# Optimization experiments

Hardware: AMD Instinct MI355X
Metric: run time of the kernel (lower is better)

The kernel has to match this reference:

```python
import jax, jax.numpy as jnp
import numpy as np

C_IN, C_OUT, H = 8, 8, 16
N1D = 20                      # 1D quadrature points -> 400 mesh nodes in 2D
B = 16
DECAY = (N1D / 4.0) ** 4      # set_quad: decay_param = (N/4)**4


def _quad_mesh():
    # Gauss-Legendre nodes/weights on [-1,1], tensor-product in 2D (get_quad_mesh)
    x, w = np.polynomial.legendre.leggauss(N1D)
    X, Y = np.meshgrid(x, x, indexing='xy')
    WX, WY = np.meshgrid(w, w, indexing='xy')
    nodes = np.dstack([X, Y]).reshape(-1, 2).astype(np.float32)
    weights = (WX * WY).reshape(-1).astype(np.float32)
    return nodes, weights


def setup_inputs() -> dict:
    key = jax.random.key(0)
    k1, k2, k3, k4 = jax.random.split(key, 4)
    nodes, w = _quad_mesh()
    K = C_IN * C_OUT
    return {
        'features': jax.random.normal(k1, (B, C_IN, N1D * N1D), jnp.float32),
        # 64 tiny MLPs (Linear no bias + Sin), spec (2,16,16,1), stacked on axis 0
        'W1': jax.random.normal(k2, (K, H, 2), jnp.float32) / np.sqrt(2.0),
        'W2': jax.random.normal(k3, (K, H, H), jnp.float32) / np.sqrt(float(H)),
        'W3': jax.random.normal(k4, (K, 1, H), jnp.float32) / np.sqrt(float(H)),
        'output_locs': jnp.asarray(nodes),   # (M,2) same tensor-product mesh
        'mesh_nodes': jnp.asarray(nodes),    # (N,2)
        'mesh_weights': jnp.asarray(w),      # (N,) product of 1D weights
    }


def _kernel(W1, W2, W3, output_locs, mesh_nodes):
    # pairwise eval points z = y_m - x_n, shape (M, N, 2)
    z = output_locs[:, None, :] - mesh_nodes[None, :, :]
    M, N, _ = z.shape
    zf = z.reshape(M * N, 2)
    # batched tiny MLPs: Linear -> Sin -> Linear -> Sin -> Linear (no bias)
    h = jnp.sin(jnp.einsum('khd,pd->kph', W1, zf))
    h = jnp.sin(jnp.einsum('koh,kph->kpo', W2, h))
    kv = jnp.einsum('koh,kph->kpo', W3, h)[..., 0]          # (K, M*N)
    # bump function enforcing compact support: exp(1 - 1/(1 - c*||z||^4))
    bump_arg = jnp.sum(zf * zf, axis=-1) ** 2               # ||z||^4
    inside = bump_arg < 1.0 / DECAY
    safe = jnp.where(inside, 1.0 - DECAY * bump_arg, 1.0)
    bump = jnp.where(inside, jnp.exp(1.0 - 1.0 / safe), 0.0)
    kv = kv * bump[None, :]
    return kv.reshape(C_OUT, C_IN, M, N)


def reference(features, W1, W2, W3, output_locs, mesh_nodes, mesh_weights):
    Kmat = _kernel(W1, W2, W3, output_locs, mesh_nodes)     # (Co,Ci,M,N)
    # quadrature-weighted conv sum: out[b,o,m] = sum_{i,n} K[o,i,m,n] w[n] f[b,i,n]
    return jnp.einsum('oimn,n,bin->bom', Kmat, mesh_weights, features)
```

## Files before the change

kernel.cpp:

```cpp
#include <hip/hip_runtime.h>
#include <math.h>

#define CIN   8
#define COUT  8
#define HH    16
#define NN    400
#define MM    400
#define BB    16

#define THREADS 512
#define GM      2
#define PMAX    32

#define WS_FT 0
#define WS_L  (NN*CIN*BB)

__global__ __launch_bounds__(THREADS) void prep_kernel(
    const float* __restrict__ f,
    const float* __restrict__ locs,
    const float* __restrict__ nodes,
    const float* __restrict__ wq,
    float* __restrict__ ws)
{
    const int blk = blockIdx.x;
    const int t   = threadIdx.x;

    if (blk < 100) {
        int idx = blk * 512 + t;
        int b = idx / 3200;
        int r = idx - b * 3200;
        int i = r / 400;
        int n = r - i * 400;
        ws[WS_FT + n*128 + i*16 + b] = f[idx];
    } else {
        const int lane = t & 63;
        const int w    = t >> 6;
        const int m    = (blk - 100) * 8 + w;
        const float2 y = ((const float2*)locs)[m];
        const float2* nd = (const float2*)nodes;
        float4* lst = (float4*)(ws + WS_L);
        int cnt = 0;
        for (int n0 = 0; n0 < NN; n0 += 64) {
            int n = n0 + lane;
            bool in = false;
            float zx = 0.f, zy = 0.f, bwv = 0.f;
            if (n < NN) {
                float2 x = nd[n];
                zx = y.x - x.x; zy = y.y - x.y;
                float s = zx*zx + zy*zy;
                float a = s * s;
                if (a < (1.0f/625.0f)) {
                    in = true;
                    bwv = __expf(1.0f - 1.0f/(1.0f - 625.0f*a)) * wq[n];
                }
            }
            unsigned long long msk = __ballot(in);
            int idx = cnt + __popcll(msk & ((1ull << lane) - 1ull));
            if (in && idx < PMAX)
                lst[m*PMAX + idx] = make_float4(zx, zy, bwv, __int_as_float(n));
            cnt += __popcll(msk);
        }
        if (lane >= cnt && lane < PMAX)
            lst[m*PMAX + lane] = make_float4(0.f, 0.f, 0.f, __int_as_float(0));
    }
}

__global__ __launch_bounds__(THREADS, 4) void quadconv_kernel(
    const float* __restrict__ W1,
    const float* __restrict__ W2,
    const float* __restrict__ W3,
    const float* __restrict__ ws,
    float* __restrict__ out)
{
    __shared__ float s_w2[8*256];
    __shared__ float s_w1[8*32];
    __shared__ float s_w3[8*16];
    __shared__ float s_kv[8*64];
    __shared__ float s_part[8*32];
    __shared__ int   s_pn[64];

    const int t    = threadIdx.x;
    const int lane = t & 63;
    const int w    = __builtin_amdgcn_readfirstlane(t >> 6);
    const int pg   = blockIdx.x >> 3;
    const int kg   = blockIdx.x & 7;
    const int m0   = pg * GM;

    {
        const float4* W2v = (const float4*)(W2 + kg * 8 * 256);
        ((float4*)s_w2)[t] = W2v[t];
        if (t < 64) ((float4*)s_w1)[t] = ((const float4*)(W1 + kg * 8 * 32))[t];
        if (t < 32) ((float4*)s_w3)[t] = ((const float4*)(W3 + kg * 8 * 16))[t];
    }

    const float4 sv = ((const float4*)(ws + WS_L))[pg*64 + lane];
    if (t < 64) s_pn[t] = __float_as_int(sv.w);
    __syncthreads();

    {
        const float* __restrict__ w1 = s_w1 + w * 32;
        const float* __restrict__ w2 = s_w2 + w * 256;
        const float* __restrict__ w3 = s_w3 + w * 16;
        const float zx = sv.x, zy = sv.y, bw = sv.z;

        float h1[HH];
        #pragma unroll
        for (int j = 0; j < HH; ++j)
            h1[j] = __sinf(w1[2*j] * zx + w1[2*j + 1] * zy);

        float kv = 0.f;
        #pragma unroll
        for (int oo = 0; oo < HH; ++oo) {
            float d = 0.f;
            #pragma unroll
            for (int j = 0; j < HH; ++j)
                d += w2[oo*HH + j] * h1[j];
            kv += w3[oo] * __sinf(d);
        }
        s_kv[w*64 + lane] = kv * bw;
    }
    __syncthreads();

    {
        const int b    = lane & 15;
        const int g    = (lane >> 4) & 1;
        const int half = lane >> 5;
        const float* __restrict__ ftp = ws + WS_FT;
        float acc = 0.f;
        #pragma unroll
        for (int jj = 0; jj < PMAX/2; ++jj) {
            int   sl = g*PMAX + half*(PMAX/2) + jj;
            int   n  = s_pn[sl];
            acc += s_kv[w*64 + sl] * ftp[n*128 + w*16 + b];
        }
        acc += __shfl_xor(acc, 32);
        if (half == 0)
            s_part[w*32 + lane] = acc;
    }
    __syncthreads();

    if (t < 32) {
        const int b = t & 15, g = t >> 4;
        float v = 0.f;
        #pragma unroll
        for (int ww = 0; ww < 8; ++ww)
            v += s_part[ww*32 + t];
        out[b * (COUT*MM) + kg * MM + (m0 + g)] = v;
    }
}

extern "C" void kernel_launch(void* const* d_in, const int* in_sizes, int n_in,
                              void* d_out, int out_size, void* d_ws, size_t ws_size,
                              hipStream_t stream) {
    const float* f     = (const float*)d_in[0];
    const float* W1    = (const float*)d_in[1];
    const float* W2    = (const float*)d_in[2];
    const float* W3    = (const float*)d_in[3];
    const float* locs  = (const float*)d_in[4];
    const float* nodes = (const float*)d_in[5];
    const float* wq    = (const float*)d_in[6];
    float* out = (float*)d_out;
    float* ws  = (float*)d_ws;

    prep_kernel<<<dim3(150), dim3(THREADS), 0, stream>>>(f, locs, nodes, wq, ws);
    quadconv_kernel<<<dim3((MM/GM) * COUT), dim3(THREADS), 0, stream>>>(
        W1, W2, W3, ws, out);
}
```

Before: 23.35 us.

## Pack variable-length support lists into 64-lane pages to cut wasted MLP evaluations

```diff
diff --git a/kernel.cpp b/kernel.cpp
--- a/kernel.cpp
+++ b/kernel.cpp
@@ -9,11 +9,24 @@
 #define BB    16
 
 #define THREADS 512
-#define GM      2
 #define PMAX    32
-
-#define WS_FT 0
-#define WS_L  (NN*CIN*BB)
+#define NGRP    16
+#define MPG     25
+#define PPG     16
+#define NPAGES  (NGRP*PPG)
+#define MAXNM   12
+
+#define WS_FT   0
+#define WS_L    (NN*CIN*BB)
+#define WS_CNT  (WS_L + MM*PMAX*4)
+#define WS_PM0  (WS_CNT + MM)
+#define WS_PNM  (WS_PM0 + NPAGES)
+
+__device__ __forceinline__ bool bump_inside(float zx, float zy, float& a) {
+    float s = __fadd_rn(__fmul_rn(zx, zx), __fmul_rn(zy, zy));
+    a = __fmul_rn(s, s);
+    return a < (1.0f / 625.0f);
+}
 
 __global__ __launch_bounds__(THREADS) void prep_kernel(
     const float* __restrict__ f,
@@ -32,7 +45,7 @@
         int i = r / 400;
         int n = r - i * 400;
         ws[WS_FT + n*128 + i*16 + b] = f[idx];
-    } else {
+    } else if (blk < 150) {
         const int lane = t & 63;
         const int w    = t >> 6;
         const int m    = (blk - 100) * 8 + w;
@@ -47,9 +60,8 @@
             if (n < NN) {
                 float2 x = nd[n];
                 zx = y.x - x.x; zy = y.y - x.y;
-                float s = zx*zx + zy*zy;
-                float a = s * s;
-                if (a < (1.0f/625.0f)) {
+                float a;
+                if (bump_inside(zx, zy, a)) {
                     in = true;
                     bwv = __expf(1.0f - 1.0f/(1.0f - 625.0f*a)) * wq[n];
                 }
@@ -62,10 +74,54 @@
         }
         if (lane >= cnt && lane < PMAX)
             lst[m*PMAX + lane] = make_float4(0.f, 0.f, 0.f, __int_as_float(0));
-    }
-}
-
-__global__ __launch_bounds__(THREADS, 4) void quadconv_kernel(
+    } else {
+        __shared__ float dx2[400], dy2[400];
+        __shared__ int   scnt[400];
+        if (t < 400) {
+            int i = t / 20, j = t % 20;
+            float zx = locs[2*i]          - nodes[2*j];
+            float zy = locs[2*(i*20) + 1] - nodes[2*(j*20) + 1];
+            dx2[t] = __fmul_rn(zx, zx);
+            dy2[t] = __fmul_rn(zy, zy);
+        }
+        __syncthreads();
+        if (t < 400) {
+            int mx = t % 20, my = t / 20;
+            int c = 0;
+            for (int ny = 0; ny < 20; ++ny) {
+                float dyv = dy2[my*20 + ny];
+                for (int nx = 0; nx < 20; ++nx) {
+                    float s = __fadd_rn(dx2[mx*20 + nx], dyv);
+                    float a = __fmul_rn(s, s);
+                    c += (a < (1.0f / 625.0f)) ? 1 : 0;
+                }
+            }
+            c = min(c, PMAX);
+            scnt[t] = c;
+            ((int*)ws)[WS_CNT + t] = c;
+        }
+        __syncthreads();
+        if (t < NGRP) {
+            int* pm0 = (int*)ws + WS_PM0;
+            int* pnm = (int*)ws + WS_PNM;
+            const int m0g = t * MPG, mend = m0g + MPG;
+            int p = t * PPG;
+            int cur0 = m0g, used = 0;
+            for (int m = m0g; m < mend; ++m) {
+                int c = scnt[m];
+                if (used + c > 64) {
+                    pm0[p] = cur0; pnm[p] = m - cur0; ++p;
+                    cur0 = m; used = 0;
+                }
+                used += c;
+            }
+            pm0[p] = cur0; pnm[p] = mend - cur0; ++p;
+            for (; p < (t + 1) * PPG; ++p) { pm0[p] = 0; pnm[p] = 0; }
+        }
+    }
+}
+
+__global__ __launch_bounds__(THREADS) void quadconv_kernel(
     const float* __restrict__ W1,
     const float* __restrict__ W2,
     const float* __restrict__ W3,
@@ -76,15 +132,18 @@
     __shared__ float s_w1[8*32];
     __shared__ float s_w3[8*16];
     __shared__ float s_kv[8*64];
-    __shared__ float s_part[8*32];
     __shared__ int   s_pn[64];
+    __shared__ int   s_off[MAXNM + 1];
+    __shared__ int   s_m0;
 
     const int t    = threadIdx.x;
     const int lane = t & 63;
     const int w    = __builtin_amdgcn_readfirstlane(t >> 6);
-    const int pg   = blockIdx.x >> 3;
+    const int p    = blockIdx.x >> 3;
     const int kg   = blockIdx.x & 7;
-    const int m0   = pg * GM;
+
+    const int nm = ((const int*)ws)[WS_PNM + p];
+    if (nm == 0) return;
 
     {
         const float4* W2v = (const float4*)(W2 + kg * 8 * 256);
@@ -92,10 +151,32 @@
         if (t < 64) ((float4*)s_w1)[t] = ((const float4*)(W1 + kg * 8 * 32))[t];
         if (t < 32) ((float4*)s_w3)[t] = ((const float4*)(W3 + kg * 8 * 16))[t];
     }
-
-    const float4 sv = ((const float4*)(ws + WS_L))[pg*64 + lane];
-    if (t < 64) s_pn[t] = __float_as_int(sv.w);
+    if (t == 0) {
+        int m0 = ((const int*)ws)[WS_PM0 + p];
+        s_m0 = m0;
+        int off = 0;
+        s_off[0] = 0;
+        for (int j = 0; j < nm; ++j) {
+            off += ((const int*)ws)[WS_CNT + m0 + j];
+            s_off[j + 1] = off;
+        }
+    }
     __syncthreads();
+
+    int seg = 0;
+    #pragma unroll
+    for (int sgi = 1; sgi < MAXNM; ++sgi)
+        seg += (sgi < nm && lane >= s_off[sgi]) ? 1 : 0;
+    const int used = s_off[nm];
+    float4 sv = make_float4(0.f, 0.f, 0.f, 0.f);
+    int n_id = 0;
+    if (lane < used) {
+        const int m  = s_m0 + seg;
+        const int jj = lane - s_off[seg];
+        sv = ((const float4*)(ws + WS_L))[m * PMAX + jj];
+        n_id = __float_as_int(sv.w);
+    }
+    if (t < 64) s_pn[t] = n_id;
 
     {
         const float* __restrict__ w1 = s_w1 + w * 32;
@@ -121,31 +202,21 @@
     }
     __syncthreads();
 
-    {
-        const int b    = lane & 15;
-        const int g    = (lane >> 4) & 1;
-        const int half = lane >> 5;
+    if (t < nm * 16) {
+        const int b    = t & 15;
+        const int sidx = t >> 4;
+        const int lo   = s_off[sidx];
+        const int L    = s_off[sidx + 1] - lo;
         const float* __restrict__ ftp = ws + WS_FT;
         float acc = 0.f;
-        #pragma unroll
-        for (int jj = 0; jj < PMAX/2; ++jj) {
-            int   sl = g*PMAX + half*(PMAX/2) + jj;
-            int   n  = s_pn[sl];
-            acc += s_kv[w*64 + sl] * ftp[n*128 + w*16 + b];
-        }
-        acc += __shfl_xor(acc, 32);
-        if (half == 0)
-            s_part[w*32 + lane] = acc;
-    }
-    __syncthreads();
-
-    if (t < 32) {
-        const int b = t & 15, g = t >> 4;
-        float v = 0.f;
-        #pragma unroll
-        for (int ww = 0; ww < 8; ++ww)
-            v += s_part[ww*32 + t];
-        out[b * (COUT*MM) + kg * MM + (m0 + g)] = v;
+        for (int j = 0; j < L; ++j) {
+            const int n = s_pn[lo + j];
+            const float* fb = ftp + n*128 + b;
+            #pragma unroll
+            for (int ww = 0; ww < 8; ++ww)
+                acc += s_kv[ww*64 + lo + j] * fb[ww*16];
+        }
+        out[b * (COUT*MM) + kg * MM + (s_m0 + sidx)] = acc;
     }
 }
 
@@ -162,7 +233,7 @@
     float* out = (float*)d_out;
     float* ws  = (float*)d_ws;
 
-    prep_kernel<<<dim3(150), dim3(THREADS), 0, stream>>>(f, locs, nodes, wq, ws);
-    quadconv_kernel<<<dim3((MM/GM) * COUT), dim3(THREADS), 0, stream>>>(
+    prep_kernel<<<dim3(151), dim3(THREADS), 0, stream>>>(f, locs, nodes, wq, ws);
+    quadconv_kernel<<<dim3(NPAGES * 8), dim3(THREADS), 0, stream>>>(
         W1, W2, W3, ws, out);
 }
```

Result: slower. 26.80 us (+14.8%).
